# Kernel tuning notes

Measured on AMD Instinct MI355X. Metric: run time of the kernel, lower is better.

The kernel has to match this reference:

```python
import jax, jax.numpy as jnp
import numpy as np

B, C, H, W = 32, 17, 96, 72
K = 3
DIL = 1
PAD = (K // 2) * DIL
KK = K * K


def setup_inputs() -> dict:
    key = jax.random.key(0)
    k1, k2, k3, k4, k5 = jax.random.split(key, 5)
    x = jax.random.normal(k1, (B, C, H, W), jnp.float32)
    offsets = jax.random.normal(k2, (B, 2 * C * KK, H, W), jnp.float32)
    mask = jax.random.uniform(k3, (B, C * KK, H, W), jnp.float32)
    # depthwise conv: weight [C_out=C, C_in/groups=1, K, K], bias [C]
    weight = jax.random.normal(k4, (C, 1, K, K), jnp.float32) * 0.1
    bias = jax.random.normal(k5, (C,), jnp.float32) * 0.01
    return {"x": x, "offsets": offsets, "mask": mask, "weight": weight, "bias": bias}


def _deform_conv(x, offsets, mask, weight, bias):
    # Modulated deformable conv (DCNv2), depthwise, offset_groups == channels.
    off = offsets.reshape(B, C, KK, 2, H, W)
    dy = off[:, :, :, 0]  # [B,C,KK,H,W]
    dx = off[:, :, :, 1]
    m = mask.reshape(B, C, KK, H, W)

    ky, kx = jnp.meshgrid(jnp.arange(K), jnp.arange(K), indexing="ij")
    ky = ky.reshape(KK)
    kx = kx.reshape(KK)
    hh = jnp.arange(H)
    ww = jnp.arange(W)
    # base sampling grid [KK,H,W]
    base_y = (-PAD + ky[:, None, None] * DIL + hh[None, :, None] + 0 * ww[None, None, :]).astype(jnp.float32)
    base_x = (-PAD + kx[:, None, None] * DIL + 0 * hh[None, :, None] + ww[None, None, :]).astype(jnp.float32)

    py = base_y[None, None] + dy  # [B,C,KK,H,W]
    px = base_x[None, None] + dx

    y0f = jnp.floor(py)
    x0f = jnp.floor(px)
    wy = py - y0f
    wx = px - x0f
    y0 = y0f.astype(jnp.int32)
    x0 = x0f.astype(jnp.int32)

    img = x.reshape(B, C, H * W)

    def corner(yi, xi, w):
        # zero-padding semantics: out-of-bounds corners contribute 0
        valid = (yi >= 0) & (yi < H) & (xi >= 0) & (xi < W)
        idx = jnp.clip(yi, 0, H - 1) * W + jnp.clip(xi, 0, W - 1)
        v = jnp.take_along_axis(img, idx.reshape(B, C, -1), axis=2).reshape(B, C, KK, H, W)
        return v * jnp.where(valid, w, 0.0)

    val = (corner(y0, x0, (1 - wy) * (1 - wx))
           + corner(y0, x0 + 1, (1 - wy) * wx)
           + corner(y0 + 1, x0, wy * (1 - wx))
           + corner(y0 + 1, x0 + 1, wy * wx))

    out = jnp.einsum("bckhw,ck->bchw", val * m, weight.reshape(C, KK))
    return out + bias[None, :, None, None]


def reference(x, offsets, mask, weight, bias):
    return _deform_conv(x, offsets, mask, weight, bias)
```

## Files before the change

### kernel.cpp

```cpp
#include <hip/hip_runtime.h>

#define Bn   32
#define Cn   17
#define Hn   96
#define Wn   72
#define Kn   3
#define KKn  9
#define PADn 1
#define HWn  (Hn * Wn)
#define TPB  384
#define PX_PER_BLOCK (TPB * 2)
#define NBLK_X (HWn / PX_PER_BLOCK)

__global__ __launch_bounds__(TPB) void deform_conv_kernel(
    const float* __restrict__ x,
    const float* __restrict__ offsets,
    const float* __restrict__ mask,
    const float* __restrict__ weight,
    const float* __restrict__ bias,
    float* __restrict__ out)
{
    __shared__ float xs[HWn];

    const int tid = threadIdx.x;
    const int bc  = blockIdx.y;
    const int c   = bc % Cn;

    {
        const float2* __restrict__ xp2 = (const float2*)(x + (size_t)bc * HWn);
        float2* xs2 = (float2*)xs;
        #pragma unroll
        for (int j = 0; j < HWn / 2 / TPB; ++j) {
            const int i = j * TPB + tid;
            xs2[i] = xp2[i];
        }
    }
    __syncthreads();

    const int hw = blockIdx.x * PX_PER_BLOCK + tid * 2;
    const int h  = hw / Wn;
    const int w  = hw - h * Wn;

    const float* __restrict__ offp = offsets + (size_t)bc * (KKn * 2 * HWn) + hw;
    const float* __restrict__ mp   = mask    + (size_t)bc * (KKn * HWn) + hw;
    const float* __restrict__ wp   = weight  + c * KKn;

    const float bv = bias[c];
    float acc0 = bv, acc1 = bv;

    #pragma unroll
    for (int kk = 0; kk < KKn; ++kk) {
        const float2 dy2 = *(const float2*)(offp + (size_t)(kk * 2 + 0) * HWn);
        const float2 dx2 = *(const float2*)(offp + (size_t)(kk * 2 + 1) * HWn);
        const float2 m2  = *(const float2*)(mp + (size_t)kk * HWn);
        const float  wk  = wp[kk];

        const int ky = kk / Kn;
        const int kx = kk - ky * Kn;
        const float base_y = (float)(h - PADn + ky);

        #pragma unroll
        for (int p = 0; p < 2; ++p) {
            const float dy = p ? dy2.y : dy2.x;
            const float dx = p ? dx2.y : dx2.x;
            const float m  = p ? m2.y  : m2.x;

            const float py = base_y + dy;
            const float px = (float)(w + p - PADn + kx) + dx;

            const float y0f = floorf(py);
            const float x0f = floorf(px);
            const float wy  = py - y0f;
            const float wx  = px - x0f;
            const int y0 = (int)y0f;
            const int x0 = (int)x0f;
            const int y1 = y0 + 1;
            const int x1 = x0 + 1;

            const int y0c = min(max(y0, 0), Hn - 1);
            const int y1c = min(max(y1, 0), Hn - 1);
            const int x0c = min(max(x0, 0), Wn - 1);
            const int x1c = min(max(x1, 0), Wn - 1);

            const float wy0 = (y0 == y0c) ? (1.f - wy) : 0.f;
            const float wy1 = (y1 == y1c) ? wy         : 0.f;
            const float wx0 = (x0 == x0c) ? (1.f - wx) : 0.f;
            const float wx1 = (x1 == x1c) ? wx         : 0.f;

            const int r0 = y0c * Wn;
            const int r1 = y1c * Wn;
            const float row0 = xs[r0 + x0c] * wx0 + xs[r0 + x1c] * wx1;
            const float row1 = xs[r1 + x0c] * wx0 + xs[r1 + x1c] * wx1;
            const float v    = row0 * wy0 + row1 * wy1;

            const float mw = m * wk;
            if (p) acc1 += v * mw; else acc0 += v * mw;
        }
    }

    float2 o; o.x = acc0; o.y = acc1;
    *(float2*)(out + (size_t)bc * HWn + hw) = o;
}

extern "C" void kernel_launch(void* const* d_in, const int* in_sizes, int n_in,
                              void* d_out, int out_size, void* d_ws, size_t ws_size,
                              hipStream_t stream) {
    const float* x       = (const float*)d_in[0];
    const float* offsets = (const float*)d_in[1];
    const float* mask    = (const float*)d_in[2];
    const float* weight  = (const float*)d_in[3];
    const float* bias    = (const float*)d_in[4];
    float* out = (float*)d_out;

    dim3 block(TPB, 1, 1);
    dim3 grid(NBLK_X, Bn * Cn, 1);
    deform_conv_kernel<<<grid, block, 0, stream>>>(x, offsets, mask, weight, bias, out);
}
```

Baseline: 460.2 us.

## Process 4 strided rows per thread with larger blocks to amortize LDS image load

```diff
diff --git a/kernel.cpp b/kernel.cpp
--- a/kernel.cpp
+++ b/kernel.cpp
@@ -8,9 +8,11 @@
 #define KKn  9
 #define PADn 1
 #define HWn  (Hn * Wn)
-#define TPB  384
-#define PX_PER_BLOCK (TPB * 2)
-#define NBLK_X (HWn / PX_PER_BLOCK)
+#define TPB  576
+#define ROWS_PER_BLOCK 32
+#define PX_PER_BLOCK (ROWS_PER_BLOCK * Wn)
+#define NBLK_X (Hn / ROWS_PER_BLOCK)
+#define NPX  4
 
 __global__ __launch_bounds__(TPB) void deform_conv_kernel(
     const float* __restrict__ x,
@@ -27,46 +29,49 @@
     const int c   = bc % Cn;
 
     {
-        const float2* __restrict__ xp2 = (const float2*)(x + (size_t)bc * HWn);
-        float2* xs2 = (float2*)xs;
+        const float4* __restrict__ xp4 = (const float4*)(x + (size_t)bc * HWn);
+        float4* xs4 = (float4*)xs;
         #pragma unroll
-        for (int j = 0; j < HWn / 2 / TPB; ++j) {
+        for (int j = 0; j < HWn / 4 / TPB; ++j) {
             const int i = j * TPB + tid;
-            xs2[i] = xp2[i];
+            xs4[i] = xp4[i];
         }
     }
     __syncthreads();
 
-    const int hw = blockIdx.x * PX_PER_BLOCK + tid * 2;
-    const int h  = hw / Wn;
-    const int w  = hw - h * Wn;
+    const int w  = tid % Wn;
+    const int h0 = blockIdx.x * ROWS_PER_BLOCK + tid / Wn;
 
-    const float* __restrict__ offp = offsets + (size_t)bc * (KKn * 2 * HWn) + hw;
-    const float* __restrict__ mp   = mask    + (size_t)bc * (KKn * HWn) + hw;
+    const float* __restrict__ offp = offsets + (size_t)bc * (KKn * 2 * HWn);
+    const float* __restrict__ mp   = mask    + (size_t)bc * (KKn * HWn);
     const float* __restrict__ wp   = weight  + c * KKn;
 
     const float bv = bias[c];
-    float acc0 = bv, acc1 = bv;
+    float acc[NPX] = {bv, bv, bv, bv};
+
+    const int hw0 = h0 * Wn + w;
 
     #pragma unroll
     for (int kk = 0; kk < KKn; ++kk) {
-        const float2 dy2 = *(const float2*)(offp + (size_t)(kk * 2 + 0) * HWn);
-        const float2 dx2 = *(const float2*)(offp + (size_t)(kk * 2 + 1) * HWn);
-        const float2 m2  = *(const float2*)(mp + (size_t)kk * HWn);
-        const float  wk  = wp[kk];
-
+        const float wk = wp[kk];
         const int ky = kk / Kn;
         const int kx = kk - ky * Kn;
-        const float base_y = (float)(h - PADn + ky);
+
+        float dyv[NPX], dxv[NPX], mv[NPX];
+        #pragma unroll
+        for (int p = 0; p < NPX; ++p) {
+            const int hw_p = hw0 + p * 8 * Wn;
+            dyv[p] = offp[(size_t)(kk * 2 + 0) * HWn + hw_p];
+            dxv[p] = offp[(size_t)(kk * 2 + 1) * HWn + hw_p];
+            mv[p]  = mp[(size_t)kk * HWn + hw_p];
+        }
 
         #pragma unroll
-        for (int p = 0; p < 2; ++p) {
-            const float dy = p ? dy2.y : dy2.x;
-            const float dx = p ? dx2.y : dx2.x;
-            const float m  = p ? m2.y  : m2.x;
+        for (int p = 0; p < NPX; ++p) {
+            const int hp = h0 + 8 * p;
 
-            const float py = base_y + dy;
-            const float px = (float)(w + p - PADn + kx) + dx;
+            const float py = (float)(hp - PADn + ky) + dyv[p];
+            const float px = (float)(w  - PADn + kx) + dxv[p];
 
             const float y0f = floorf(py);
             const float x0f = floorf(px);
@@ -93,13 +98,15 @@
             const float row1 = xs[r1 + x0c] * wx0 + xs[r1 + x1c] * wx1;
             const float v    = row0 * wy0 + row1 * wy1;
 
-            const float mw = m * wk;
-            if (p) acc1 += v * mw; else acc0 += v * mw;
+            acc[p] += v * (mv[p] * wk);
         }
     }
 
-    float2 o; o.x = acc0; o.y = acc1;
-    *(float2*)(out + (size_t)bc * HWn + hw) = o;
+    const size_t ob = (size_t)bc * HWn;
+    #pragma unroll
+    for (int p = 0; p < NPX; ++p) {
+        out[ob + hw0 + p * 8 * Wn] = acc[p];
+    }
 }
 
 extern "C" void kernel_launch(void* const* d_in, const int* in_sizes, int n_in,
```

Measured after the change: 459.4 us. No clear change (-0.2%).

## Process four pixels per thread with whole-image blocks, LDS padding, and prefetch

Applied to the files above, without the earlier changes.

```diff
diff --git a/kernel.cpp b/kernel.cpp
--- a/kernel.cpp
+++ b/kernel.cpp
@@ -8,9 +8,13 @@
 #define KKn  9
 #define PADn 1
 #define HWn  (Hn * Wn)
-#define TPB  384
-#define PX_PER_BLOCK (TPB * 2)
+#define TPB  576
+#define PX_PER_THREAD 4
+#define PX_PER_BLOCK (TPB * PX_PER_THREAD)
 #define NBLK_X (HWn / PX_PER_BLOCK)
+
+#define SWZ(i) ((i) + ((i) >> 5))
+#define XS_SIZE (HWn + HWn / 32)
 
 __global__ __launch_bounds__(TPB) void deform_conv_kernel(
     const float* __restrict__ x,
@@ -20,24 +24,26 @@
     const float* __restrict__ bias,
     float* __restrict__ out)
 {
-    __shared__ float xs[HWn];
+    __shared__ float xs[XS_SIZE];
 
     const int tid = threadIdx.x;
     const int bc  = blockIdx.y;
     const int c   = bc % Cn;
 
     {
-        const float2* __restrict__ xp2 = (const float2*)(x + (size_t)bc * HWn);
-        float2* xs2 = (float2*)xs;
+        const float4* __restrict__ xp4 = (const float4*)(x + (size_t)bc * HWn);
         #pragma unroll
-        for (int j = 0; j < HWn / 2 / TPB; ++j) {
-            const int i = j * TPB + tid;
-            xs2[i] = xp2[i];
+        for (int j = 0; j < HWn / 4 / TPB; ++j) {
+            const int ci = j * TPB + tid;
+            const float4 v = xp4[ci];
+            const int i = ci * 4;
+            const int s = SWZ(i);
+            xs[s + 0] = v.x; xs[s + 1] = v.y; xs[s + 2] = v.z; xs[s + 3] = v.w;
         }
     }
     __syncthreads();
 
-    const int hw = blockIdx.x * PX_PER_BLOCK + tid * 2;
+    const int hw = blockIdx.x * PX_PER_BLOCK + tid * PX_PER_THREAD;
     const int h  = hw / Wn;
     const int w  = hw - h * Wn;
 
@@ -46,24 +52,31 @@
     const float* __restrict__ wp   = weight  + c * KKn;
 
     const float bv = bias[c];
-    float acc0 = bv, acc1 = bv;
+    float acc[PX_PER_THREAD] = {bv, bv, bv, bv};
+
+    float4 dy4 = *(const float4*)(offp + 0 * HWn);
+    float4 dx4 = *(const float4*)(offp + 1 * HWn);
+    float4 m4  = *(const float4*)(mp   + 0 * HWn);
 
     #pragma unroll
     for (int kk = 0; kk < KKn; ++kk) {
-        const float2 dy2 = *(const float2*)(offp + (size_t)(kk * 2 + 0) * HWn);
-        const float2 dx2 = *(const float2*)(offp + (size_t)(kk * 2 + 1) * HWn);
-        const float2 m2  = *(const float2*)(mp + (size_t)kk * HWn);
-        const float  wk  = wp[kk];
+        float4 ndy, ndx, nm;
+        if (kk < KKn - 1) {
+            ndy = *(const float4*)(offp + (size_t)(kk * 2 + 2) * HWn);
+            ndx = *(const float4*)(offp + (size_t)(kk * 2 + 3) * HWn);
+            nm  = *(const float4*)(mp   + (size_t)(kk + 1) * HWn);
+        }
 
+        const float wk = wp[kk];
         const int ky = kk / Kn;
         const int kx = kk - ky * Kn;
         const float base_y = (float)(h - PADn + ky);
 
         #pragma unroll
-        for (int p = 0; p < 2; ++p) {
-            const float dy = p ? dy2.y : dy2.x;
-            const float dx = p ? dx2.y : dx2.x;
-            const float m  = p ? m2.y  : m2.x;
+        for (int p = 0; p < PX_PER_THREAD; ++p) {
+            const float dy = ((const float*)&dy4)[p];
+            const float dx = ((const float*)&dx4)[p];
+            const float m  = ((const float*)&m4)[p];
 
             const float py = base_y + dy;
             const float px = (float)(w + p - PADn + kx) + dx;
@@ -89,17 +102,24 @@
 
             const int r0 = y0c * Wn;
             const int r1 = y1c * Wn;
-            const float row0 = xs[r0 + x0c] * wx0 + xs[r0 + x1c] * wx1;
-            const float row1 = xs[r1 + x0c] * wx0 + xs[r1 + x1c] * wx1;
+            const float v00 = xs[SWZ(r0 + x0c)];
+            const float v01 = xs[SWZ(r0 + x1c)];
+            const float v10 = xs[SWZ(r1 + x0c)];
+            const float v11 = xs[SWZ(r1 + x1c)];
+
+            const float row0 = v00 * wx0 + v01 * wx1;
+            const float row1 = v10 * wx0 + v11 * wx1;
             const float v    = row0 * wy0 + row1 * wy1;
 
-            const float mw = m * wk;
-            if (p) acc1 += v * mw; else acc0 += v * mw;
+            acc[p] += v * (m * wk);
         }
+
+        dy4 = ndy; dx4 = ndx; m4 = nm;
     }
 
-    float2 o; o.x = acc0; o.y = acc1;
-    *(float2*)(out + (size_t)bc * HWn + hw) = o;
+    float4 o;
+    o.x = acc[0]; o.y = acc[1]; o.z = acc[2]; o.w = acc[3];
+    *(float4*)(out + (size_t)bc * HWn + hw) = o;
 }
 
 extern "C" void kernel_launch(void* const* d_in, const int* in_sizes, int n_in,
```

After: 471.6 us. 2.5% more time.
